# Kernel tuning notes

Measured on AMD Instinct MI355X. Metric: run time of the kernel, lower is better.

The kernel has to match this reference:

```python
import jax, jax.numpy as jnp
import numpy as np

E = 384      # EMBEDDING_SIZE
DFF = 1536
H = 6        # NUM_HEADS
D = E // H   # ATTN_DIM_SIZE = 64
T = 256      # SEQ_LEN
L = 6        # NUM_BLOCKS
V = 65       # VOCAB_SIZE
NPOS = 10000.0
B = 128


def _pos_encoding():
    i = jnp.arange(T, dtype=jnp.float32)[:, None]
    k = jnp.arange(E // 2, dtype=jnp.float32)[None, :]
    ang = i / jnp.power(NPOS, 2.0 * k / E)   # [T, E/2]
    pe = jnp.zeros((T, E), dtype=jnp.float32)
    pe = pe.at[:, 0::2].set(jnp.sin(ang))
    pe = pe.at[:, 1::2].set(jnp.cos(ang))
    return pe


def setup_inputs() -> dict:
    key = jax.random.key(0)
    ks = jax.random.split(key, 24)
    s = 0.02
    n = lambda k, shp: (jax.random.normal(k, shp, dtype=jnp.float32) * s)
    inp = {
        'tokens': jax.random.randint(ks[0], (B, T), 0, V),
        'pos_enc': _pos_encoding(),
        'emb': n(ks[1], (V, E)),
        # stacked per-layer params [L, ...]; weights stored as (in, out)
        'Wq': n(ks[2], (L, E, E)), 'bq': jnp.zeros((L, E)),
        'Wk': n(ks[3], (L, E, E)), 'bk': jnp.zeros((L, E)),
        'Wv': n(ks[4], (L, E, E)), 'bv': jnp.zeros((L, E)),
        'Wo': n(ks[5], (L, E, E)), 'bo': jnp.zeros((L, E)),
        'ln1_g': jnp.ones((L, E)), 'ln1_b': jnp.zeros((L, E)),
        'W1': n(ks[6], (L, E, DFF)), 'c1': jnp.zeros((L, DFF)),
        'W2': n(ks[7], (L, DFF, E)), 'c2': jnp.zeros((L, E)),
        'ln2_g': jnp.ones((L, E)), 'ln2_b': jnp.zeros((L, E)),
        'Wl': n(ks[8], (E, V)), 'bl': jnp.zeros((V,)),
    }
    return inp


def _layer_norm(x, g, b, eps=1e-5):
    mu = jnp.mean(x, axis=-1, keepdims=True)
    var = jnp.mean((x - mu) ** 2, axis=-1, keepdims=True)
    return (x - mu) * jax.lax.rsqrt(var + eps) * g + b


def _decoder(tokens, pos_enc, emb, Wq, bq, Wk, bk, Wv, bv, Wo, bo,
             ln1_g, ln1_b, W1, c1, W2, c2, ln2_g, ln2_b, Wl, bl):
    b_, t_ = tokens.shape
    x = emb[tokens] + pos_enc[None, :t_, :]            # [B,T,E]
    causal = jnp.tril(jnp.ones((t_, t_), dtype=bool)) # tril mask
    scale = D ** (-0.5)

    def block(x, p):
        (wq, bq_, wk, bk_, wv, bv_, wo, bo_, g1, be1, w1, c1_, w2, c2_, g2, be2) = p
        h = _layer_norm(x, g1, be1)
        q = (h @ wq + bq_).reshape(b_, t_, H, D)
        k = (h @ wk + bk_).reshape(b_, t_, H, D)
        v = (h @ wv + bv_).reshape(b_, t_, H, D)
        scores = jnp.einsum('bqhd,bkhd->bhqk', q, k) * scale
        scores = jnp.where(causal[None, None], scores, -jnp.inf)
        attn = jax.nn.softmax(scores, axis=-1)
        o = jnp.einsum('bhqk,bkhd->bqhd', attn, v).reshape(b_, t_, E)
        x = x + (o @ wo + bo_)
        h2 = _layer_norm(x, g2, be2)
        x = x + (jax.nn.relu(h2 @ w1 + c1_) @ w2 + c2_)
        return x, None

    params = (Wq, bq, Wk, bk, Wv, bv, Wo, bo, ln1_g, ln1_b, W1, c1, W2, c2, ln2_g, ln2_b)
    x, _ = jax.lax.scan(block, x, params)
    return x @ Wl + bl                                 # [B,T,V]


def reference(tokens, pos_enc, emb, Wq, bq, Wk, bk, Wv, bv, Wo, bo,
              ln1_g, ln1_b, W1, c1, W2, c2, ln2_g, ln2_b, Wl, bl):
    return _decoder(tokens, pos_enc, emb, Wq, bq, Wk, bk, Wv, bv, Wo, bo,
                    ln1_g, ln1_b, W1, c1, W2, c2, ln2_g, ln2_b, Wl, bl)
```

## Files before the change

### kernel.cpp

```cpp
#include <hip/hip_runtime.h>
#include <hip/hip_bf16.h>
#include <stdint.h>

constexpr int E   = 384;
constexpr int DFF = 1536;
constexpr int NH  = 6;
constexpr int HD  = 64;
constexpr int T   = 256;
constexpr int NL  = 6;
constexpr int NV  = 65;
constexpr int BB  = 128;
constexpr int MTOT = BB * T;
constexpr int CB  = 32;

typedef __bf16 bf16;
typedef __attribute__((ext_vector_type(8))) __bf16 bf16x8;
typedef __attribute__((ext_vector_type(4))) __bf16 bf16x4;
typedef __attribute__((ext_vector_type(4))) float floatx4;

__device__ __forceinline__ void gload_lds16(const void* g, void* l) {
    __builtin_amdgcn_global_load_lds(
        (const __attribute__((address_space(1))) void*)g,
        (__attribute__((address_space(3))) void*)l, 16, 0, 0);
}

#define GBN 128

template <int MODE, int SWAP, int W>
__device__ __forceinline__ void gemm_body(
    char* AsB,
    const bf16* __restrict__ A, int lda,
    const bf16* __restrict__ Bf,
    const float* __restrict__ bias,
    void* __restrict__ Cv, void* __restrict__ Cv2, int ldc,
    int nt, int mt, int Nvalid, int K, int relu)
{
    constexpr int BM     = W * 32;
    constexpr int ABYTES = BM * 64;
    constexpr int SBUF   = ABYTES + 8192;

    int tid = threadIdx.x;
    int lane = tid & 63;
    int wid = tid >> 6;
    int wr = wid >> 1, wc = wid & 1;
    int lq = lane >> 4, lr = lane & 15;

    const bf16* Ab = A + (long)mt * BM * lda;

    int rp0 = wid * 8 + (lane >> 3);
    int s   = lane & 7;
    int sp  = s ^ (rp0 & 7);
    int rowA = 2 * rp0 + (sp >> 2);
    int kOff = (sp & 3) * 8;
    const bf16* srcA0 = Ab + (long)rowA * lda + kOff;
    const bf16* srcA1 = srcA0 + (long)(BM / 2) * lda;
    int dst0 = wid * 1024;
    int dst1 = W * 1024 + wid * 1024;

    int nks = K / 32;

    const bf16* srcB0;
    const bf16* srcB1 = nullptr;
    int dstB0, dstB1 = 0;
    if constexpr (W == 8) {
        srcB0 = Bf + ((long)(nt * 8 + wid) * nks) * 512 + lane * 8;
        dstB0 = ABYTES + wid * 1024;
    } else {
        srcB0 = Bf + ((long)(nt * 8 + wid * 2) * nks) * 512 + lane * 8;
        srcB1 = Bf + ((long)(nt * 8 + wid * 2 + 1) * nks) * 512 + lane * 8;
        dstB0 = ABYTES + (wid * 2) * 1024;
        dstB1 = ABYTES + (wid * 2 + 1) * 1024;
    }

    floatx4 acc[4][4];
#pragma unroll
    for (int i = 0; i < 4; i++)
#pragma unroll
        for (int j = 0; j < 4; j++) acc[i][j] = floatx4{0.f, 0.f, 0.f, 0.f};

    int afo = (wr * 32 + (lr >> 1)) * 128 +
              (((((lr & 1) << 2) | lq) ^ (lr >> 1)) << 4);
    int bfo = ABYTES + wc * 4096 + lane * 16;

    auto stage = [&](int ks, int bo) {
        long ka = (long)ks * 32;
        gload_lds16(srcA0 + ka, AsB + bo + dst0);
        gload_lds16(srcA1 + ka, AsB + bo + dst1);
        long kb = (long)ks * 512;
        gload_lds16(srcB0 + kb, AsB + bo + dstB0);
        if constexpr (W == 4)
            gload_lds16(srcB1 + kb, AsB + bo + dstB1);
    };

    int o0 = 0, o1 = SBUF, o2 = 2 * SBUF;

    stage(0, o0);
    if (nks > 1) {
        stage(1, o1);
        if constexpr (W == 8)
            asm volatile("s_waitcnt vmcnt(3)" ::: "memory");
        else
            asm volatile("s_waitcnt vmcnt(4)" ::: "memory");
    } else {
        asm volatile("s_waitcnt vmcnt(0)" ::: "memory");
    }
    __builtin_amdgcn_s_barrier();

    for (int ki = 0; ki < nks; ++ki) {
        if (ki + 2 < nks) stage(ki + 2, o2);
        __builtin_amdgcn_sched_barrier(0);

        bf16x8 bfr[4];
#pragma unroll
        for (int ni = 0; ni < 4; ni++)
            bfr[ni] = *(const bf16x8*)(AsB + o0 + bfo + ni * 1024);
        bf16x8 af[4];
#pragma unroll
        for (int mi = 0; mi < 4; mi++)
            af[mi] = *(const bf16x8*)(AsB + o0 + afo + mi * 1024);

        __builtin_amdgcn_s_setprio(1);
#pragma unroll
        for (int mi = 0; mi < 4; mi++)
#pragma unroll
            for (int ni = 0; ni < 4; ni++)
                acc[mi][ni] = SWAP
                    ? __builtin_amdgcn_mfma_f32_16x16x32_bf16(bfr[ni], af[mi], acc[mi][ni], 0, 0, 0)
                    : __builtin_amdgcn_mfma_f32_16x16x32_bf16(af[mi], bfr[ni], acc[mi][ni], 0, 0, 0);
        __builtin_amdgcn_s_setprio(0);

        if (ki + 1 < nks) {
            if (ki + 2 < nks) {
                if constexpr (W == 8)
                    asm volatile("s_waitcnt vmcnt(3) lgkmcnt(0)" ::: "memory");
                else
                    asm volatile("s_waitcnt vmcnt(4) lgkmcnt(0)" ::: "memory");
            } else {
                asm volatile("s_waitcnt vmcnt(0) lgkmcnt(0)" ::: "memory");
            }
            __builtin_amdgcn_s_barrier();
        }
        int t = o0; o0 = o1; o1 = o2; o2 = t;
    }

    int m0 = mt * BM, n0 = nt * GBN;
#pragma unroll
    for (int mi = 0; mi < 4; mi++) {
#pragma unroll
        for (int ni = 0; ni < 4; ni++) {
            floatx4 v = acc[mi][ni];
            if (SWAP) {
                int rowL = m0 + wr * 64 + mi * 16 + lr;
                int col0 = n0 + wc * 64 + ni * 16 + lq * 4;
                if (MODE == 5) {
                    bf16x4 pv;
#pragma unroll
                    for (int r = 0; r < 4; r++) pv[r] = (bf16)(v[r] + bias[col0 + r]);
                    *(bf16x4*)((bf16*)Cv + (long)rowL * 768 + col0) = pv;
                } else if (MODE == 1) {
                    bf16* Cp = (bf16*)Cv;
                    bf16x4* ptr = (bf16x4*)(Cp + (long)rowL * ldc + col0);
                    bf16x4 old = *ptr;
                    bf16x4 pv;
#pragma unroll
                    for (int r = 0; r < 4; r++)
                        pv[r] = (bf16)((float)old[r] + v[r] + bias[col0 + r]);
                    *ptr = pv;
                } else if (MODE == 4) {
                    float* Cp = (float*)Cv;
#pragma unroll
                    for (int r = 0; r < 4; r++)
                        if (col0 + r < Nvalid)
                            Cp[(long)rowL * ldc + col0 + r] = v[r] + bias[col0 + r];
                } else {
                    if (col0 < Nvalid) {
                        bf16x4 pv;
#pragma unroll
                        for (int r = 0; r < 4; r++) {
                            float x = v[r] + (bias ? bias[col0 + r] : 0.f);
                            if (relu) x = fmaxf(x, 0.f);
                            pv[r] = (bf16)x;
                        }
                        *(bf16x4*)((bf16*)Cv + (long)rowL * ldc + col0) = pv;
                    }
                }
            } else {
                int row0 = m0 + wr * 64 + mi * 16 + lq * 4;
                int colL = n0 + wc * 64 + ni * 16 + lr;
                float bv = bias[colL];
                bf16x4 pv;
#pragma unroll
                for (int r = 0; r < 4; r++) pv[r] = (bf16)(v[r] + bv);
                int bidx = row0 >> 8, pos = row0 & 255, e = colL - 768;
                *(bf16x4*)((bf16*)Cv2 + (long)bidx * (E * T) + (long)e * T + pos) = pv;
            }
        }
    }
}

template <int MODE, int W>
__global__ __launch_bounds__(W * 64, 4) void k_gemm(
    const bf16* __restrict__ A, int lda,
    const bf16* __restrict__ Bf,
    const float* __restrict__ bias,
    void* __restrict__ Cv, void* __restrict__ Cv2, int ldc,
    int Mtiles, int Ntiles, int Nvalid, int K,
    int relu)
{
    __shared__ __align__(16) char AsB[3 * (W * 32 * 64 + 8192)];

    int nb = gridDim.x;
    int per = nb >> 3;
    int bphys = blockIdx.x;
    int bid = (bphys & 7) * per + (bphys >> 3);

    int nt = bid % Ntiles;
    int mt = bid / Ntiles;

    if (MODE == 5 && nt >= 6)
        gemm_body<5, 0, W>(AsB, A, lda, Bf, bias, Cv, Cv2, ldc, nt, mt, Nvalid, K, relu);
    else
        gemm_body<MODE, 1, W>(AsB, A, lda, Bf, bias, Cv, Cv2, ldc, nt, mt, Nvalid, K, relu);
}

__global__ __launch_bounds__(256) void k_attn(
    const bf16* __restrict__ qk, const bf16* __restrict__ vt,
    bf16* __restrict__ o)
{
    int nb = gridDim.x;
    int per = nb >> 3;
    int bphys = blockIdx.x;
    int bid = (bphys & 7) * per + (bphys >> 3);

    int qt = bid & 3; bid >>= 2;
    int h = bid % NH; int b = bid / NH;
    int tid = threadIdx.x;
    int lane = tid & 63;
    int w = tid >> 6;
    int lq = lane >> 4;
    int lr = lane & 15;

    __shared__ __align__(16) bf16 Ks[256 * 72];
    __shared__ __align__(16) bf16 Vs[64 * 264];

    const bf16* qbase = qk + (long)(b * T + qt * 64 + w * 16) * 768 + h * 64;
    const bf16* kbase = qk + (long)(b * T) * 768 + 384 + h * 64;
    const bf16* vbase = vt + ((long)b * E + h * 64) * T;

#pragma unroll
    for (int i = 0; i < 8; i++) {
        int idx = i * 256 + tid;
        int row = idx >> 3, off = (idx & 7) * 8;
        *(bf16x8*)(&Ks[row * 72 + off]) = *(const bf16x8*)(kbase + (long)row * 768 + off);
    }
#pragma unroll
    for (int i = 0; i < 8; i++) {
        int idx = i * 256 + tid;
        int row = idx >> 5, off = (idx & 31) * 8;
        *(bf16x8*)(&Vs[row * 264 + off]) = *(const bf16x8*)(vbase + (long)row * 256 + off);
    }

    bf16x8 aq0 = *(const bf16x8*)(qbase + (long)lr * 768 + lq * 8);
    bf16x8 aq1 = *(const bf16x8*)(qbase + (long)lr * 768 + 32 + lq * 8);

    __syncthreads();

    const int ntmax = qt * 4 + 3;
    floatx4 zero = {0.f, 0.f, 0.f, 0.f};
    floatx4 s[16];
#pragma unroll
    for (int nt = 0; nt < 16; nt++) s[nt] = zero;

#pragma unroll
    for (int nt = 0; nt < 16; nt++) {
        if (nt <= ntmax) {
            const bf16* kp = &Ks[(nt * 16 + lr) * 72 + lq * 8];
            bf16x8 b0 = *(const bf16x8*)(kp);
            bf16x8 b1 = *(const bf16x8*)(kp + 32);
            s[nt] = __builtin_amdgcn_mfma_f32_16x16x32_bf16(aq0, b0, s[nt], 0, 0, 0);
            s[nt] = __builtin_amdgcn_mfma_f32_16x16x32_bf16(aq1, b1, s[nt], 0, 0, 0);
        }
    }

    int trow0 = qt * 64 + w * 16 + lq * 4;
    float m4[4] = {-3e38f, -3e38f, -3e38f, -3e38f};
#pragma unroll
    for (int nt = 0; nt < 16; nt++) {
        if (nt <= ntmax) {
            int tc = nt * 16 + lr;
#pragma unroll
            for (int r = 0; r < 4; r++) {
                float v = s[nt][r] * 0.125f;
                if (tc > trow0 + r) v = -3e38f;
                s[nt][r] = v;
                m4[r] = fmaxf(m4[r], v);
            }
        }
    }
#pragma unroll
    for (int r = 0; r < 4; r++) {
#pragma unroll
        for (int off = 1; off < 16; off <<= 1)
            m4[r] = fmaxf(m4[r], __shfl_xor(m4[r], off, 64));
    }

    float l4[4] = {0.f, 0.f, 0.f, 0.f};
#pragma unroll
    for (int nt = 0; nt < 16; nt++) {
        if (nt <= ntmax) {
#pragma unroll
            for (int r = 0; r < 4; r++) {
                float pv = __expf(s[nt][r] - m4[r]);
                l4[r] += pv;
                s[nt][r] = pv;
            }
        }
    }
#pragma unroll
    for (int r = 0; r < 4; r++) {
#pragma unroll
        for (int off = 1; off < 16; off <<= 1)
            l4[r] += __shfl_xor(l4[r], off, 64);
    }

    __syncthreads();

    bf16* P = Ks + w * (16 * 264);
#pragma unroll
    for (int nt = 0; nt < 16; nt++) {
        if (nt <= ntmax) {
#pragma unroll
            for (int r = 0; r < 4; r++)
                P[(lq * 4 + r) * 264 + nt * 16 + lr] = (bf16)s[nt][r];
        }
    }

    floatx4 oacc[4];
#pragma unroll
    for (int nd = 0; nd < 4; nd++) oacc[nd] = zero;
    const int kkmax = 2 * (qt + 1);
#pragma unroll
    for (int kk = 0; kk < 8; kk++) {
        if (kk < kkmax) {
            bf16x8 ap = *(const bf16x8*)(&P[lr * 264 + kk * 32 + lq * 8]);
#pragma unroll
            for (int nd = 0; nd < 4; nd++) {
                bf16x8 bv = *(const bf16x8*)(&Vs[(nd * 16 + lr) * 264 + kk * 32 + lq * 8]);
                oacc[nd] = __builtin_amdgcn_mfma_f32_16x16x32_bf16(ap, bv, oacc[nd], 0, 0, 0);
            }
        }
    }

#pragma unroll
    for (int r = 0; r < 4; r++) {
        float inv = 1.0f / l4[r];
        long rowg = (long)b * T + trow0 + r;
#pragma unroll
        for (int nd = 0; nd < 4; nd++) {
            o[rowg * E + h * 64 + nd * 16 + lr] = (bf16)(oacc[nd][r] * inv);
        }
    }
}

__global__ void k_ln(const bf16* __restrict__ x, const float* __restrict__ g,
                     const float* __restrict__ b, bf16* __restrict__ h) {
    int row = blockIdx.x * 4 + (threadIdx.x >> 6);
    int lane = threadIdx.x & 63;
    const bf16* xr = x + (long)row * E;
    float v[6];
    float s = 0.f;
#pragma unroll
    for (int i = 0; i < 6; i++) { v[i] = (float)xr[lane + 64 * i]; s += v[i]; }
#pragma unroll
    for (int o = 1; o < 64; o <<= 1) s += __shfl_xor(s, o, 64);
    float mu = s * (1.0f / E);
    float q = 0.f;
#pragma unroll
    for (int i = 0; i < 6; i++) { float d = v[i] - mu; q += d * d; }
#pragma unroll
    for (int o = 1; o < 64; o <<= 1) q += __shfl_xor(q, o, 64);
    float rs = rsqrtf(q * (1.0f / E) + 1e-5f);
    bf16* hr = h + (long)row * E;
#pragma unroll
    for (int i = 0; i < 6; i++) {
        int c = lane + 64 * i;
        hr[c] = (bf16)((v[i] - mu) * rs * g[c] + b[c]);
    }
}

__global__ void k_transpose_frag(const float* __restrict__ W, bf16* __restrict__ Wf,
                                 int K, int N, int NPAD) {
    long idx = (long)blockIdx.x * 256 + threadIdx.x;
    long per = (long)NPAD * K;
    int l = (int)(idx / per);
    long r = idx - (long)l * per;
    int j = (int)(r & 7); r >>= 3;
    int lane = (int)(r & 63); r >>= 6;
    int nks = K / 32;
    int ks = (int)(r % nks);
    int c16 = (int)(r / nks);
    int col = c16 * 16 + (lane & 15);
    int k = ks * 32 + (lane >> 4) * 8 + j;
    Wf[idx] = (col < N) ? (bf16)W[((long)l * K + k) * N + col] : (bf16)0.0f;
}

__global__ void k_transpose_qkv_frag(const float* __restrict__ Wq, const float* __restrict__ Wk,
                                     const float* __restrict__ Wv, bf16* __restrict__ Wf) {
    long idx = (long)blockIdx.x * 256 + threadIdx.x;
    long per = (long)1152 * E;
    int l = (int)(idx / per);
    long r = idx - (long)l * per;
    int j = (int)(r & 7); r >>= 3;
    int lane = (int)(r & 63); r >>= 6;
    int nks = E / 32;
    int ks = (int)(r % nks);
    int c16 = (int)(r / nks);
    int col = c16 * 16 + (lane & 15);
    int k = ks * 32 + (lane >> 4) * 8 + j;
    const float* src;
    int cc;
    if (col < 384)      { src = Wq; cc = col; }
    else if (col < 768) { src = Wk; cc = col - 384; }
    else                { src = Wv; cc = col - 768; }
    Wf[idx] = (bf16)src[((long)l * E + k) * E + cc];
}

__global__ void k_bias_qkv(const float* __restrict__ bq, const float* __restrict__ bk,
                           const float* __restrict__ bv, float* __restrict__ bqkv) {
    int idx = blockIdx.x * 256 + threadIdx.x;
    int l = idx / 1152;
    int j = idx - l * 1152;
    const float* src;
    int jj;
    if (j < 384)      { src = bq; jj = j; }
    else if (j < 768) { src = bk; jj = j - 384; }
    else              { src = bv; jj = j - 768; }
    bqkv[idx] = src[l * E + jj];
}

__global__ void k_embed(const int* __restrict__ tokens, const float* __restrict__ pos,
                        const float* __restrict__ emb, bf16* __restrict__ x) {
    long idx = (long)blockIdx.x * 256 + threadIdx.x;
    int e = (int)(idx % E);
    long bt = idx / E;
    int t = (int)(bt % T);
    int tok = tokens[bt];
    x[idx] = (bf16)(emb[(long)tok * E + e] + pos[(long)t * E + e]);
}

extern "C" void kernel_launch(void* const* d_in, const int* in_sizes, int n_in,
                              void* d_out, int out_size, void* d_ws, size_t ws_size,
                              hipStream_t stream) {
    const int*   tokens = (const int*)d_in[0];
    const float* pos  = (const float*)d_in[1];
    const float* emb  = (const float*)d_in[2];
    const float* Wq   = (const float*)d_in[3];
    const float* bq   = (const float*)d_in[4];
    const float* Wk   = (const float*)d_in[5];
    const float* bk   = (const float*)d_in[6];
    const float* Wv   = (const float*)d_in[7];
    const float* bv   = (const float*)d_in[8];
    const float* Wo   = (const float*)d_in[9];
    const float* bo   = (const float*)d_in[10];
    const float* g1   = (const float*)d_in[11];
    const float* be1  = (const float*)d_in[12];
    const float* W1   = (const float*)d_in[13];
    const float* c1   = (const float*)d_in[14];
    const float* W2   = (const float*)d_in[15];
    const float* c2   = (const float*)d_in[16];
    const float* g2   = (const float*)d_in[17];
    const float* be2  = (const float*)d_in[18];
    const float* Wl   = (const float*)d_in[19];
    const float* bl   = (const float*)d_in[20];

    char* p = (char*)d_ws;
    bf16* x  = (bf16*)p;   p += (long)MTOT * E * 2;
    bf16* h  = (bf16*)p;   p += (long)MTOT * E * 2;
    bf16* qk = (bf16*)p;   p += (long)MTOT * 768 * 2;
    bf16* vt = (bf16*)p;   p += (long)BB * E * T * 2;
    bf16* SP = (bf16*)p;   p += (long)CB * NH * T * T * 2;
    bf16* WqkvF = (bf16*)p; p += (long)NL * 1152 * E * 2;
    bf16* WoF = (bf16*)p;  p += (long)NL * E * E * 2;
    bf16* W1F = (bf16*)p;  p += (long)NL * DFF * E * 2;
    bf16* W2F = (bf16*)p;  p += (long)NL * E * DFF * 2;
    bf16* WlF = (bf16*)p;  p += (long)128 * E * 2;
    float* bqkv = (float*)p; p += (long)NL * 1152 * 4;
    bf16* mid = qk;
    bf16* o   = h;
    (void)SP;

    k_transpose_qkv_frag<<<(NL * 1152 * E) / 256, 256, 0, stream>>>(Wq, Wk, Wv, WqkvF);
    k_transpose_frag<<<(NL * E * E) / 256, 256, 0, stream>>>(Wo, WoF, E, E, E);
    k_transpose_frag<<<(NL * DFF * E) / 256, 256, 0, stream>>>(W1, W1F, E, DFF, DFF);
    k_transpose_frag<<<(NL * E * DFF) / 256, 256, 0, stream>>>(W2, W2F, DFF, E, E);
    k_transpose_frag<<<(128 * E) / 256, 256, 0, stream>>>(Wl, WlF, E, NV, 128);
    k_bias_qkv<<<(NL * 1152) / 256, 256, 0, stream>>>(bq, bk, bv, bqkv);

    k_embed<<<(MTOT * E) / 256, 256, 0, stream>>>(tokens, pos, emb, x);

    for (int l = 0; l < NL; l++) {
        k_ln<<<MTOT / 4, 256, 0, stream>>>(x, g1 + l * E, be1 + l * E, h);
        k_gemm<5, 8><<<128 * 9, 512, 0, stream>>>(h, E, WqkvF + (long)l * 1152 * E,
                                                  bqkv + l * 1152, qk, vt, 0,
                                                  128, 9, 1152, E, 0);
        k_attn<<<BB * NH * 4, 256, 0, stream>>>(qk, vt, o);
        k_gemm<1, 4><<<256 * 3, 256, 0, stream>>>(o, E, WoF + (long)l * E * E,
                                                  bo + l * E, x, nullptr, E,
                                                  256, 3, E, E, 0);
        k_ln<<<MTOT / 4, 256, 0, stream>>>(x, g2 + l * E, be2 + l * E, h);
        k_gemm<0, 8><<<128 * 12, 512, 0, stream>>>(h, E, W1F + (long)l * DFF * E,
                                                   c1 + l * DFF, mid, nullptr, DFF,
                                                   128, 12, DFF, E, 1);
        k_gemm<1, 4><<<256 * 3, 256, 0, stream>>>(mid, DFF, W2F + (long)l * E * DFF,
                                                  c2 + l * E, x, nullptr, E,
                                                  256, 3, E, DFF, 0);
    }

    k_gemm<4, 4><<<256 * 1, 256, 0, stream>>>(x, E, WlF,
                                              bl, d_out, nullptr, NV,
                                              256, 1, NV, E, 0);
}
```

Measured before the change: 1.701 ms.

## Fold LayerNorm into following GEMMs via row stats and weight prescaling

```diff
diff --git a/kernel.cpp b/kernel.cpp
--- a/kernel.cpp
+++ b/kernel.cpp
@@ -33,7 +33,8 @@
     const bf16* __restrict__ Bf,
     const float* __restrict__ bias,
     void* __restrict__ Cv, void* __restrict__ Cv2, int ldc,
-    int nt, int mt, int Nvalid, int K, int relu)
+    int nt, int mt, int Nvalid, int K, int relu,
+    const float2* __restrict__ st, const float* __restrict__ uvec)
 {
     constexpr int BM     = W * 32;
     constexpr int ABYTES = BM * 64;
@@ -153,10 +154,24 @@
                 int rowL = m0 + wr * 64 + mi * 16 + lr;
                 int col0 = n0 + wc * 64 + ni * 16 + lq * 4;
                 if (MODE == 5) {
+                    float2 s2 = st[rowL];
                     bf16x4 pv;
 #pragma unroll
-                    for (int r = 0; r < 4; r++) pv[r] = (bf16)(v[r] + bias[col0 + r]);
+                    for (int r = 0; r < 4; r++)
+                        pv[r] = (bf16)(s2.y * v[r] - s2.x * uvec[col0 + r] + bias[col0 + r]);
                     *(bf16x4*)((bf16*)Cv + (long)rowL * 768 + col0) = pv;
+                } else if (MODE == 2) {
+                    if (col0 < Nvalid) {
+                        float2 s2 = st[rowL];
+                        bf16x4 pv;
+#pragma unroll
+                        for (int r = 0; r < 4; r++) {
+                            float x = s2.y * v[r] - s2.x * uvec[col0 + r] + bias[col0 + r];
+                            if (relu) x = fmaxf(x, 0.f);
+                            pv[r] = (bf16)x;
+                        }
+                        *(bf16x4*)((bf16*)Cv + (long)rowL * ldc + col0) = pv;
+                    }
                 } else if (MODE == 1) {
                     bf16* Cp = (bf16*)Cv;
                     bf16x4* ptr = (bf16x4*)(Cp + (long)rowL * ldc + col0);
@@ -187,10 +202,14 @@
             } else {
                 int row0 = m0 + wr * 64 + mi * 16 + lq * 4;
                 int colL = n0 + wc * 64 + ni * 16 + lr;
-                float bv = bias[colL];
+                float uu = uvec[colL];
+                float cc = bias[colL];
                 bf16x4 pv;
 #pragma unroll
-                for (int r = 0; r < 4; r++) pv[r] = (bf16)(v[r] + bv);
+                for (int r = 0; r < 4; r++) {
+                    float2 s2 = st[row0 + r];
+                    pv[r] = (bf16)(s2.y * v[r] - s2.x * uu + cc);
+                }
                 int bidx = row0 >> 8, pos = row0 & 255, e = colL - 768;
                 *(bf16x4*)((bf16*)Cv2 + (long)bidx * (E * T) + (long)e * T + pos) = pv;
             }
@@ -205,7 +224,8 @@
     const float* __restrict__ bias,
     void* __restrict__ Cv, void* __restrict__ Cv2, int ldc,
     int Mtiles, int Ntiles, int Nvalid, int K,
-    int relu)
+    int relu,
+    const float2* __restrict__ st, const float* __restrict__ uvec)
 {
     __shared__ __align__(16) char AsB[3 * (W * 32 * 64 + 8192)];
 
@@ -218,9 +238,9 @@
     int mt = bid / Ntiles;
 
     if (MODE == 5 && nt >= 6)
-        gemm_body<5, 0, W>(AsB, A, lda, Bf, bias, Cv, Cv2, ldc, nt, mt, Nvalid, K, relu);
+        gemm_body<5, 0, W>(AsB, A, lda, Bf, bias, Cv, Cv2, ldc, nt, mt, Nvalid, K, relu, st, uvec);
     else
-        gemm_body<MODE, 1, W>(AsB, A, lda, Bf, bias, Cv, Cv2, ldc, nt, mt, Nvalid, K, relu);
+        gemm_body<MODE, 1, W>(AsB, A, lda, Bf, bias, Cv, Cv2, ldc, nt, mt, Nvalid, K, relu, st, uvec);
 }
 
 __global__ __launch_bounds__(256) void k_attn(
@@ -362,8 +382,7 @@
     }
 }
 
-__global__ void k_ln(const bf16* __restrict__ x, const float* __restrict__ g,
-                     const float* __restrict__ b, bf16* __restrict__ h) {
+__global__ void k_stats(const bf16* __restrict__ x, float2* __restrict__ st) {
     int row = blockIdx.x * 4 + (threadIdx.x >> 6);
     int lane = threadIdx.x & 63;
     const bf16* xr = x + (long)row * E;
@@ -380,16 +399,11 @@
 #pragma unroll
     for (int o = 1; o < 64; o <<= 1) q += __shfl_xor(q, o, 64);
     float rs = rsqrtf(q * (1.0f / E) + 1e-5f);
-    bf16* hr = h + (long)row * E;
-#pragma unroll
-    for (int i = 0; i < 6; i++) {
-        int c = lane + 64 * i;
-        hr[c] = (bf16)((v[i] - mu) * rs * g[c] + b[c]);
-    }
-}
-
-__global__ void k_transpose_frag(const float* __restrict__ W, bf16* __restrict__ Wf,
-                                 int K, int N, int NPAD) {
+    if (lane == 0) st[row] = make_float2(mu * rs, rs);
+}
+
+__global__ void k_transpose_frag(const float* __restrict__ W, const float* __restrict__ g,
+                                 bf16* __restrict__ Wf, int K, int N, int NPAD) {
     long idx = (long)blockIdx.x * 256 + threadIdx.x;
     long per = (long)NPAD * K;
     int l = (int)(idx / per);
@@ -401,11 +415,13 @@
     int c16 = (int)(r / nks);
     int col = c16 * 16 + (lane & 15);
     int k = ks * 32 + (lane >> 4) * 8 + j;
-    Wf[idx] = (col < N) ? (bf16)W[((long)l * K + k) * N + col] : (bf16)0.0f;
+    float sc = g ? g[(long)l * K + k] : 1.0f;
+    Wf[idx] = (col < N) ? (bf16)(W[((long)l * K + k) * N + col] * sc) : (bf16)0.0f;
 }
 
 __global__ void k_transpose_qkv_frag(const float* __restrict__ Wq, const float* __restrict__ Wk,
-                                     const float* __restrict__ Wv, bf16* __restrict__ Wf) {
+                                     const float* __restrict__ Wv, const float* __restrict__ g1,
+                                     bf16* __restrict__ Wf) {
     long idx = (long)blockIdx.x * 256 + threadIdx.x;
     long per = (long)1152 * E;
     int l = (int)(idx / per);
@@ -422,20 +438,44 @@
     if (col < 384)      { src = Wq; cc = col; }
     else if (col < 768) { src = Wk; cc = col - 384; }
     else                { src = Wv; cc = col - 768; }
-    Wf[idx] = (bf16)src[((long)l * E + k) * E + cc];
-}
-
-__global__ void k_bias_qkv(const float* __restrict__ bq, const float* __restrict__ bk,
-                           const float* __restrict__ bv, float* __restrict__ bqkv) {
+    Wf[idx] = (bf16)(src[((long)l * E + k) * E + cc] * g1[(long)l * E + k]);
+}
+
+__global__ void k_colconst_qkv(const float* __restrict__ Wq, const float* __restrict__ Wk,
+                               const float* __restrict__ Wv, const float* __restrict__ g,
+                               const float* __restrict__ bb,
+                               const float* __restrict__ bq, const float* __restrict__ bk,
+                               const float* __restrict__ bv,
+                               float* __restrict__ u, float* __restrict__ cv) {
     int idx = blockIdx.x * 256 + threadIdx.x;
-    int l = idx / 1152;
-    int j = idx - l * 1152;
-    const float* src;
-    int jj;
-    if (j < 384)      { src = bq; jj = j; }
-    else if (j < 768) { src = bk; jj = j - 384; }
-    else              { src = bv; jj = j - 768; }
-    bqkv[idx] = src[l * E + jj];
+    int l = idx / 1152, n = idx - l * 1152;
+    const float* W; const float* bsrc; int cc;
+    if (n < 384)      { W = Wq; bsrc = bq; cc = n; }
+    else if (n < 768) { W = Wk; bsrc = bk; cc = n - 384; }
+    else              { W = Wv; bsrc = bv; cc = n - 768; }
+    float su = 0.f, sw = 0.f;
+    for (int c = 0; c < E; c++) {
+        float w = W[((long)l * E + c) * E + cc];
+        su += g[(long)l * E + c] * w;
+        sw += bb[(long)l * E + c] * w;
+    }
+    u[idx] = su;
+    cv[idx] = sw + bsrc[(long)l * E + cc];
+}
+
+__global__ void k_colconst(const float* __restrict__ W, const float* __restrict__ g,
+                           const float* __restrict__ bb, const float* __restrict__ bias,
+                           float* __restrict__ u, float* __restrict__ cv, int K, int N) {
+    int idx = blockIdx.x * 256 + threadIdx.x;
+    int l = idx / N, n = idx - l * N;
+    float su = 0.f, sw = 0.f;
+    for (int c = 0; c < K; c++) {
+        float w = W[((long)l * K + c) * N + n];
+        su += g[(long)l * K + c] * w;
+        sw += bb[(long)l * K + c] * w;
+    }
+    u[idx] = su;
+    cv[idx] = sw + bias[idx];
 }
 
 __global__ void k_embed(const int* __restrict__ tokens, const float* __restrict__ pos,
@@ -484,39 +524,48 @@
     bf16* W1F = (bf16*)p;  p += (long)NL * DFF * E * 2;
     bf16* W2F = (bf16*)p;  p += (long)NL * E * DFF * 2;
     bf16* WlF = (bf16*)p;  p += (long)128 * E * 2;
-    float* bqkv = (float*)p; p += (long)NL * 1152 * 4;
+    float2* st1 = (float2*)p; p += (long)MTOT * 8;
+    float2* st2 = (float2*)p; p += (long)MTOT * 8;
+    float* uq  = (float*)p; p += (long)NL * 1152 * 4;
+    float* cq  = (float*)p; p += (long)NL * 1152 * 4;
+    float* u1  = (float*)p; p += (long)NL * DFF * 4;
+    float* c1v = (float*)p; p += (long)NL * DFF * 4;
     bf16* mid = qk;
     bf16* o   = h;
     (void)SP;
 
-    k_transpose_qkv_frag<<<(NL * 1152 * E) / 256, 256, 0, stream>>>(Wq, Wk, Wv, WqkvF);
-    k_transpose_frag<<<(NL * E * E) / 256, 256, 0, stream>>>(Wo, WoF, E, E, E);
-    k_transpose_frag<<<(NL * DFF * E) / 256, 256, 0, stream>>>(W1, W1F, E, DFF, DFF);
-    k_transpose_frag<<<(NL * E * DFF) / 256, 256, 0, stream>>>(W2, W2F, DFF, E, E);
-    k_transpose_frag<<<(128 * E) / 256, 256, 0, stream>>>(Wl, WlF, E, NV, 128);
-    k_bias_qkv<<<(NL * 1152) / 256, 256, 0, stream>>>(bq, bk, bv, bqkv);
+    k_transpose_qkv_frag<<<(NL * 1152 * E) / 256, 256, 0, stream>>>(Wq, Wk, Wv, g1, WqkvF);
+    k_transpose_frag<<<(NL * E * E) / 256, 256, 0, stream>>>(Wo, nullptr, WoF, E, E, E);
+    k_transpose_frag<<<(NL * DFF * E) / 256, 256, 0, stream>>>(W1, g2, W1F, E, DFF, DFF);
+    k_transpose_frag<<<(NL * E * DFF) / 256, 256, 0, stream>>>(W2, nullptr, W2F, DFF, E, E);
+    k_transpose_frag<<<(128 * E) / 256, 256, 0, stream>>>(Wl, nullptr, WlF, E, NV, 128);
+    k_colconst_qkv<<<(NL * 1152) / 256, 256, 0, stream>>>(Wq, Wk, Wv, g1, be1,
+                                                          bq, bk, bv, uq, cq);
+    k_colconst<<<(NL * DFF) / 256, 256, 0, stream>>>(W1, g2, be2, c1, u1, c1v, E, DFF);
 
     k_embed<<<(MTOT * E) / 256, 256, 0, stream>>>(tokens, pos, emb, x);
 
     for (int l = 0; l < NL; l++) {
-        k_ln<<<MTOT / 4, 256, 0, stream>>>(x, g1 + l * E, be1 + l * E, h);
-        k_gemm<5, 8><<<128 * 9, 512, 0, stream>>>(h, E, WqkvF + (long)l * 1152 * E,
-                                                  bqkv + l * 1152, qk, vt, 0,
-                                                  128, 9, 1152, E, 0);
+        k_stats<<<MTOT / 4, 256, 0, stream>>>(x, st1);
+        k_gemm<5, 8><<<128 * 9, 512, 0, stream>>>(x, E, WqkvF + (long)l * 1152 * E,
+                                                  cq + l * 1152, qk, vt, 0,
+                                                  128, 9, 1152, E, 0,
+                                                  st1, uq + l * 1152);
         k_attn<<<BB * NH * 4, 256, 0, stream>>>(qk, vt, o);
         k_gemm<1, 4><<<256 * 3, 256, 0, stream>>>(o, E, WoF + (long)l * E * E,
                                                   bo + l * E, x, nullptr, E,
-                                                  256, 3, E, E, 0);
-        k_ln<<<MTOT / 4, 256, 0, stream>>>(x, g2 + l * E, be2 + l * E, h);
-        k_gemm<0, 8><<<128 * 12, 512, 0, stream>>>(h, E, W1F + (long)l * DFF * E,
-                                                   c1 + l * DFF, mid, nullptr, DFF,
-                                                   128, 12, DFF, E, 1);
+                                                  256, 3, E, E, 0, nullptr, nullptr);
+        k_stats<<<MTOT / 4, 256, 0, stream>>>(x, st2);
+        k_gemm<2, 8><<<128 * 12, 512, 0, stream>>>(x, E, W1F + (long)l * DFF * E,
+                                                   c1v + l * DFF, mid, nullptr, DFF,
+                                                   128, 12, DFF, E, 1,
+                                                   st2, u1 + l * DFF);
         k_gemm<1, 4><<<256 * 3, 256, 0, stream>>>(mid, DFF, W2F + (long)l * E * DFF,
                                                   c2 + l * E, x, nullptr, E,
-                                                  256, 3, E, DFF, 0);
+                                                  256, 3, E, DFF, 0, nullptr, nullptr);
     }
 
     k_gemm<4, 4><<<256 * 1, 256, 0, stream>>>(x, E, WlF,
                                               bl, d_out, nullptr, NV,
-                                              256, 1, NV, E, 0);
-}
+                                              256, 1, NV, E, 0, nullptr, nullptr);
+}
```

After: 1.886 ms. 1.11x slower.
